# Optimization experiments

Measured on AMD Instinct MI355X. Metric: run time of the kernel, lower is better.

Reference implementation:

```python
import jax, jax.numpy as jnp
import numpy as np

N_HEAD = 16


def _rope_tables(T, head_dim, dtype):
    # RotaryEmbedding buffers: freqs = outer(t, inv_freq), half-dim tables [T, head_dim//2]
    inv_freq = 1.0 / (10000.0 ** (jnp.arange(0, head_dim, 2, dtype=jnp.float32) / head_dim))
    freqs = jnp.arange(T, dtype=jnp.float32)[:, None] * inv_freq[None, :]
    return jnp.cos(freqs).astype(dtype), jnp.sin(freqs).astype(dtype)


def _apply_rotary(x, cos, sin):
    # x: [B,H,T,D]; cos/sin: [T,D//2] broadcast over B,H
    d = x.shape[-1] // 2
    x1, x2 = x[..., :d], x[..., d:]
    return jnp.concatenate([x1 * cos - x2 * sin, x2 * cos + x1 * sin], axis=-1)


def setup_inputs() -> dict:
    key = jax.random.key(0)
    k1, k2, k3 = jax.random.split(key, 3)
    B, T, C = 2, 2048, 2048
    x = jax.random.normal(k1, (B, T, C), dtype=jnp.float32)
    Wqkv = jax.random.normal(k2, (C, 3 * C), dtype=jnp.float32) * (1.0 / np.sqrt(C))
    Wproj = jax.random.normal(k3, (C, C), dtype=jnp.float32) * (1.0 / np.sqrt(C))
    return {"x": x, "Wqkv": Wqkv, "Wproj": Wproj}


def reference(x, Wqkv, Wproj):
    B, T, C = x.shape
    H = N_HEAD
    D = C // H
    qkv = (x @ Wqkv).reshape(B, T, 3, H, D)
    q, k, v = qkv[:, :, 0], qkv[:, :, 1], qkv[:, :, 2]  # [B,T,H,D]
    q = jnp.transpose(q, (0, 2, 1, 3))  # [B,H,T,D]
    k = jnp.transpose(k, (0, 2, 1, 3))
    v = jnp.transpose(v, (0, 2, 1, 3))
    cos, sin = _rope_tables(T, D, x.dtype)
    q = _apply_rotary(q, cos, sin)
    k = _apply_rotary(k, cos, sin)
    scale = 1.0 / np.sqrt(D)
    scores = jnp.einsum('bhqd,bhkd->bhqk', q, k) * scale
    causal = jnp.tril(jnp.ones((T, T), dtype=bool))
    scores = jnp.where(causal, scores, jnp.finfo(scores.dtype).min)
    attn = jax.nn.softmax(scores, axis=-1)
    out = jnp.einsum('bhqk,bhkd->bhqd', attn, v)
    out = jnp.transpose(out, (0, 2, 1, 3)).reshape(B, T, C)
    return out @ Wproj
```

## Files before the change

kernel.cpp:

```cpp
#include <hip/hip_runtime.h>
#include <hip/hip_bf16.h>

typedef short s16b;
using bf16x4 = __attribute__((ext_vector_type(4))) short;
using bf16x8 = __attribute__((ext_vector_type(8))) short;
using f32x4  = __attribute__((ext_vector_type(4))) float;
using u32x4  = __attribute__((ext_vector_type(4))) unsigned;

#define DEVINL __device__ __forceinline__

DEVINL float bf2f(short u) {
    union { float f; unsigned u; } x;
    x.u = ((unsigned)(unsigned short)u) << 16;
    return x.f;
}
DEVINL short f2bf(float f) {
    unsigned u = __builtin_bit_cast(unsigned, f);
    u += 0x7FFFu + ((u >> 16) & 1u);
    return (short)(u >> 16);
}
DEVINL unsigned cvtpk(float a, float b) {
    unsigned r;
    asm("v_cvt_pk_bf16_f32 %0, %1, %2" : "=v"(r) : "v"(a), "v"(b));
    return r;
}

DEVINL f32x4 mfma16(bf16x8 a, bf16x8 b, f32x4 c) {
    return __builtin_amdgcn_mfma_f32_16x16x32_bf16(a, b, c, 0, 0, 0);
}

DEVINL void gload_lds16(const void* g, void* lds_uniform) {
    __builtin_amdgcn_global_load_lds(
        (const __attribute__((address_space(1))) char*)(const char*)g,
        (__attribute__((address_space(3))) char*)(char*)lds_uniform, 16, 0, 0);
}

DEVINL int perm32(int k) {
    return ((k >> 2) & 3) * 8 + ((k >> 4) & 1) * 4 + (k & 3);
}

DEVINL bf16x8 lds128(const s16b* base, int row, int ks, int g) {
    const char* p = (const char*)base + row * 128 + ((((ks << 2) + g) ^ (row & 7)) << 4);
    return *(const bf16x8*)p;
}
DEVINL bf16x8 lds256(const s16b* base, int row, int ds, int g) {
    const char* p = (const char*)base + row * 256 + ((((ds << 2) + g) ^ (row & 7)) << 4);
    return *(const bf16x8*)p;
}

__global__ void k_tables(float* __restrict__ ctab, float* __restrict__ stab) {
    int idx = blockIdx.x * 256 + threadIdx.x;
    int i = idx & 63, t = idx >> 6;
    float inv = powf(10000.0f, -(float)i * (1.0f / 64.0f));
    float fr = (float)t * inv;
    ctab[idx] = cosf(fr);
    stab[idx] = sinf(fr);
}

__global__ void k_cvt_x(const float* __restrict__ x, s16b* __restrict__ xb) {
    int idx = blockIdx.x * 256 + threadIdx.x;
    int p = idx * 4;
    int row = p >> 11, pc = p & 2047;
    int grp = pc >> 5, sp = pc & 31;
    int c = sp >> 3, half = (sp >> 2) & 1;
    int ksrc = grp * 32 + half * 16 + c * 4;
    float4 v = *(const float4*)(x + (size_t)row * 2048 + ksrc);
    bf16x4 o;
    o[0] = f2bf(v.x); o[1] = f2bf(v.y); o[2] = f2bf(v.z); o[3] = f2bf(v.w);
    *(bf16x4*)(xb + (size_t)row * 2048 + pc) = o;
}

__global__ void k_tcvt(const float* __restrict__ in, s16b* __restrict__ out, int R, int C) {
    __shared__ float tile[32][33];
    int tx = threadIdx.x & 31, ty = threadIdx.x >> 5;
    int c0 = blockIdx.x * 32, r0 = blockIdx.y * 32;
#pragma unroll
    for (int kk = 0; kk < 4; ++kk) {
        int r = ty + kk * 8;
        tile[r][tx] = in[(size_t)(r0 + r) * C + c0 + tx];
    }
    __syncthreads();
#pragma unroll
    for (int kk = 0; kk < 4; ++kk) {
        int r = ty + kk * 8;
        out[(size_t)(c0 + r) * R + r0 + perm32(tx)] = f2bf(tile[tx][r]);
    }
}

#define STG_B01(DB, KB)                                                        \
  gload_lds16(srcB + (KB), lds + 49152 + (DB) * 32768 + tid16);                \
  gload_lds16(srcB + 262144 + (KB), lds + 49152 + (DB) * 32768 + 8192 + tid16);
#define STG_B23(DB, KB)                                                        \
  gload_lds16(srcB + 524288 + (KB), lds + 49152 + (DB) * 32768 + 16384 + tid16); \
  gload_lds16(srcB + 786432 + (KB), lds + 49152 + (DB) * 32768 + 24576 + tid16);
#define STG_A01(DB, KB)                                                        \
  gload_lds16(srcA + (KB), lds + (DB) * 16384 + tid16);                        \
  gload_lds16(srcA + 262144 + (KB), lds + (DB) * 16384 + 8192 + tid16);

#define AF_READ(B, KS)                                                         \
    _Pragma("unroll")                                                          \
    for (int fi = 0; fi < 4; ++fi) {                                           \
      int row = (fi >> 1) * 64 + wm * 32 + (fi & 1) * 16 + r15;                \
      af[fi] = *(const bf16x8*)(lds + (B) * 16384 + row * 128                  \
               + ((((KS) * 4 + g) ^ (row & 7)) << 4));                         \
    }

#define PH4(B, KH, JH, STGC, WN)                                               \
  {                                                                            \
    if ((JH) == 0) { AF_READ(B, KH) }                                          \
    _Pragma("unroll")                                                          \
    for (int fj = 0; fj < 2; ++fj) {                                           \
      int row = (JH) * 128 + wn * 32 + fj * 16 + r15;                          \
      bfr[fj] = *(const bf16x8*)(lds + 49152 + (B) * 32768 + row * 128         \
                + ((((KH) * 4 + g) ^ (row & 7)) << 4));                        \
    }                                                                          \
    STGC                                                                       \
    if ((WN) == 6) { asm volatile("s_waitcnt vmcnt(6)" ::: "memory");          \
                     __builtin_amdgcn_sched_barrier(0); }                      \
    else if ((WN) == 0) { asm volatile("s_waitcnt vmcnt(0)" ::: "memory");     \
                     __builtin_amdgcn_sched_barrier(0); }                      \
    __builtin_amdgcn_s_barrier();                                              \
    asm volatile("s_waitcnt lgkmcnt(0)" ::: "memory");                         \
    __builtin_amdgcn_sched_barrier(0);                                         \
    __builtin_amdgcn_s_setprio(1);                                             \
    _Pragma("unroll")                                                          \
    for (int fi = 0; fi < 4; ++fi)                                             \
      _Pragma("unroll")                                                        \
      for (int fj = 0; fj < 2; ++fj)                                           \
        acc[fi][(JH) * 2 + fj] = mfma16(af[fi], bfr[fj], acc[fi][(JH) * 2 + fj]); \
    __builtin_amdgcn_s_setprio(0);                                             \
    __builtin_amdgcn_s_barrier();                                              \
    __builtin_amdgcn_sched_barrier(0);                                         \
  }

#define DO_TILE3(B, S1, S2, S3, WNL)                                           \
    PH4(B, 0, 0, S1, -1)                                                       \
    PH4(B, 0, 1, S2, -1)                                                       \
    PH4(B, 1, 0, S3, -1)                                                       \
    PH4(B, 1, 1, , WNL)

#define GEMM3_MAINLOOP(A_, B_)                                                 \
    __shared__ __attribute__((aligned(16))) char lds[147456];                  \
    const int tid = threadIdx.x;                                               \
    const int lane = tid & 63, wave = tid >> 6;                                \
    const int g = lane >> 4, r15 = lane & 15;                                  \
    const int wm = wave >> 2, wn = wave & 3;                                   \
    const int tid16 = tid << 4;                                                \
    const int rowL = tid16 >> 7;                                               \
    const int swzL = ((((tid16 >> 4) & 7) ^ (rowL & 7)) << 4);                 \
    const char* srcA = (const char*)(A_) + (size_t)(bm + rowL) * 4096 + swzL;  \
    const char* srcB = (const char*)(B_) + (size_t)(bn + rowL) * 4096 + swzL;  \
    f32x4 acc[4][4] = {};                                                      \
    bf16x8 af[4], bfr[2];                                                      \
    STG_B01(0, 0) STG_A01(0, 0) STG_B23(0, 0)                                  \
    STG_B01(1, 128) STG_A01(1, 128) STG_B23(1, 128)                            \
    asm volatile("s_waitcnt vmcnt(6)" ::: "memory");                           \
    __builtin_amdgcn_sched_barrier(0);                                         \
    __builtin_amdgcn_s_barrier();                                              \
    for (int t3 = 0; t3 < 10; ++t3) {                                          \
        const int kb2 = (3 * t3 + 2) * 128;                                    \
        const int kb3 = kb2 + 128, kb4 = kb2 + 256;                            \
        DO_TILE3(0, STG_B01(2, kb2), STG_A01(2, kb2), STG_B23(2, kb2), 6)      \
        DO_TILE3(1, STG_B01(0, kb3), STG_A01(0, kb3), STG_B23(0, kb3), 6)      \
        DO_TILE3(2, STG_B01(1, kb4), STG_A01(1, kb4), STG_B23(1, kb4), 6)      \
    }                                                                          \
    DO_TILE3(0, , , , 0)                                                       \
    DO_TILE3(1, , , , -1)

__global__ __launch_bounds__(512) void k_gemm_qkv(
    const s16b* __restrict__ A, const s16b* __restrict__ Bt,
    s16b* __restrict__ Qb, s16b* __restrict__ Kp, s16b* __restrict__ Vt,
    const float* __restrict__ ctab, const float* __restrict__ stab) {
    const int bid = blockIdx.x;
    const int xcd = bid & 7, local = bid >> 3;
    const int rr_ = local >> 5, w = local & 31;
    const int bm = ((xcd & 3) * 8 + (w >> 2)) * 128;
    const int bn = ((xcd >> 2) * 12 + rr_ * 4 + (w & 3)) * 256;
    GEMM3_MAINLOOP(A, Bt)
    const int which = bn >> 11;
    if (which < 2) {
        char* sml = (char*)lds;
#pragma unroll
        for (int i = 0; i < 4; ++i) {
#pragma unroll
            for (int j = 0; j < 4; ++j) {
                int mb0 = (i >> 1) * 64 + wm * 32 + (i & 1) * 16 + 4 * g;
                int nn = (j >> 1) * 128 + wn * 32 + (j & 1) * 16 + r15;
#pragma unroll
                for (int e = 0; e < 4; ++e) {
                    int mm = mb0 + e;
                    *(s16b*)(sml + mm * 528 + ((nn * 2) ^ ((mm & 3) << 5))) =
                        f2bf(acc[i][j][e]);
                }
            }
        }
        __syncthreads();
        const int mrow = tid >> 2, c4 = tid & 3;
        const int bb = bm >> 11;
        const int tt = (bm & 2047) + mrow;
        const char* srow = sml + mrow * 528;
        const int sw = (mrow & 3) << 5;
        bf16x8 v[8];
#pragma unroll
        for (int k = 0; k < 8; ++k) {
            int lc = c4 + 4 * k;
            v[k] = *(const bf16x8*)(srow + ((lc * 16) ^ sw));
        }
        float cs[2][8], sn[2][8];
#pragma unroll
        for (int j = 0; j < 2; ++j) {
            int d0 = 8 * c4 + 32 * j;
            const float* cp = ctab + tt * 64 + d0;
            const float* sp = stab + tt * 64 + d0;
            *(float4*)&cs[j][0] = *(const float4*)cp;
            *(float4*)&cs[j][4] = *(const float4*)(cp + 4);
            *(float4*)&sn[j][0] = *(const float4*)sp;
            *(float4*)&sn[j][4] = *(const float4*)(sp + 4);
        }
        if (which == 0) {
            const float SC = 0.12751744154f;
#pragma unroll
            for (int j = 0; j < 2; ++j)
#pragma unroll
                for (int e = 0; e < 8; ++e) { cs[j][e] *= SC; sn[j][e] *= SC; }
        }
        bf16x8 o[8];
#pragma unroll
        for (int hh = 0; hh < 2; ++hh)
#pragma unroll
            for (int j = 0; j < 2; ++j) {
                int kl = hh * 4 + j, kh = kl + 2;
                bf16x8 r1, r2;
#pragma unroll
                for (int e = 0; e < 8; ++e) {
                    float c = cs[j][e], s = sn[j][e];
                    float x1 = bf2f(v[kl][e]), x2 = bf2f(v[kh][e]);
                    r1[e] = f2bf(x1 * c - x2 * s);
                    r2[e] = f2bf(x2 * c + x1 * s);
                }
                o[kl] = r1; o[kh] = r2;
            }
        if (which == 0) {
#pragma unroll
            for (int k = 0; k < 8; ++k) {
                int lc = c4 + 4 * k;
                int ng = bn + lc * 8;
                int h = (ng >> 7) & 15, d = ng & 127;
                *(bf16x8*)(Qb + ((size_t)(bb * 16 + h) * 2048 + tt) * 128 + d) = o[k];
            }
        } else {
#pragma unroll
            for (int k = 0; k < 8; ++k) {
                int lc = c4 + 4 * k;
                int ng = bn + lc * 8;
                int h = (ng >> 7) & 15, d = ng & 127;
                size_t base = ((size_t)(bb * 16 + h) * 2048 + tt) * 128 + (d & ~31);
                int w2 = d & 31;
                bf16x4 lo, hi;
#pragma unroll
                for (int e = 0; e < 4; ++e) { lo[e] = o[k][e]; hi[e] = o[k][e + 4]; }
                *(bf16x4*)(Kp + base + perm32(w2)) = lo;
                *(bf16x4*)(Kp + base + perm32(w2 + 4)) = hi;
            }
        }
    } else {
#pragma unroll
        for (int i = 0; i < 4; ++i) {
            int m0 = bm + (i >> 1) * 64 + wm * 32 + (i & 1) * 16 + 4 * g;
            int b = m0 >> 11, t0 = m0 & 2047;
            int pt = (t0 & ~31) + perm32(t0 & 31);
#pragma unroll
            for (int j = 0; j < 4; ++j) {
                int n = bn + (j >> 1) * 128 + wn * 32 + (j & 1) * 16 + r15;
                int h = (n >> 7) & 15, d = n & 127;
                size_t base = ((size_t)(b * 16 + h) * 128 + d) * 2048 + pt;
                bf16x4 pk;
#pragma unroll
                for (int e = 0; e < 4; ++e) pk[e] = f2bf(acc[i][j][e]);
                *(bf16x4*)(Vt + base) = pk;
            }
        }
    }
}

__global__ __launch_bounds__(512) void k_gemm_proj(
    const s16b* __restrict__ A, const s16b* __restrict__ Bt, float* __restrict__ Co) {
    const int bid = blockIdx.x;
    const int xcd = bid & 7, local = bid >> 3;
    const int bm = (xcd * 4 + (local & 3)) * 128;
    const int bn = (local >> 2) * 256;
    GEMM3_MAINLOOP(A, Bt)
#pragma unroll
    for (int i = 0; i < 4; ++i) {
        int m0 = bm + (i >> 1) * 64 + wm * 32 + (i & 1) * 16 + 4 * g;
#pragma unroll
        for (int j = 0; j < 4; ++j) {
            int n = bn + (j >> 1) * 128 + wn * 32 + (j & 1) * 16 + r15;
#pragma unroll
            for (int e = 0; e < 4; ++e) Co[(size_t)(m0 + e) * 2048 + n] = acc[i][j][e];
        }
    }
}

__global__ __launch_bounds__(256) void k_attn(
    const s16b* __restrict__ Qb, const s16b* __restrict__ Kp,
    const s16b* __restrict__ Vt, s16b* __restrict__ AO) {
    __shared__ alignas(16) s16b Ks[64 * 128];
    __shared__ alignas(16) s16b Vs[128 * 64];
    const int tid = threadIdx.x;
    const int lane = tid & 63, wave = tid >> 6;
    const int g = lane >> 4, r15 = lane & 15;
    const int bh = blockIdx.x;
    const int qt = (blockIdx.y < 8) ? (15 - (int)blockIdx.y) : ((int)blockIdx.y - 8);
    const int q0 = qt * 128 + wave * 32;
    const s16b* Qg = Qb + (size_t)bh * 2048 * 128;
    const char* Kg = (const char*)(Kp + (size_t)bh * 2048 * 128);
    const char* Vg = (const char*)(Vt + (size_t)bh * 128 * 2048);

    bf16x8 qf[2][4];
#pragma unroll
    for (int qs = 0; qs < 2; ++qs)
#pragma unroll
        for (int ds = 0; ds < 4; ++ds) {
            const s16b* p = Qg + (size_t)(q0 + qs * 16 + r15) * 128 + ds * 32 + 4 * g;
            bf16x4 lo = *(const bf16x4*)p;
            bf16x4 hi = *(const bf16x4*)(p + 16);
            qf[qs][ds] = __builtin_shufflevector(lo, hi, 0, 1, 2, 3, 4, 5, 6, 7);
        }

    f32x4 ot[8][2] = {};
    float m_s[2] = {-3e38f, -3e38f};
    float l_s[2] = {0.f, 0.f};

    const int ktiles = qt * 2 + 2;
    for (int kt = 0; kt < ktiles; ++kt) {
        const int k0 = kt * 64;
        __syncthreads();
#pragma unroll
        for (int rr = 0; rr < 4; ++rr) {
            int uo = (rr * 256 + wave * 64) * 16;
            int o = uo + lane * 16;
            {
                int row = o >> 8, sl = (o >> 4) & 15;
                int sg = (sl ^ (row & 7)) << 4;
                gload_lds16(Kg + (size_t)(k0 + row) * 256 + sg, (char*)Ks + uo);
            }
            {
                int row = o >> 7, sl = (o >> 4) & 7;
                int sg = (sl ^ (row & 7)) << 4;
                gload_lds16(Vg + (size_t)row * 4096 + (size_t)k0 * 2 + sg, (char*)Vs + uo);
            }
        }
        __syncthreads();

        if (k0 <= q0 + 31) {
            f32x4 st[4][2] = {};
            __builtin_amdgcn_s_setprio(1);
#pragma unroll
            for (int ds = 0; ds < 4; ++ds) {
#pragma unroll
                for (int ks = 0; ks < 4; ++ks) {
                    bf16x8 kf = lds256(Ks, ks * 16 + r15, ds, g);
#pragma unroll
                    for (int qs = 0; qs < 2; ++qs)
                        st[ks][qs] = mfma16(kf, qf[qs][ds], st[ks][qs]);
                }
            }
            __builtin_amdgcn_s_setprio(0);
            if (k0 + 63 > q0) {
#pragma unroll
                for (int ks = 0; ks < 4; ++ks)
#pragma unroll
                    for (int qs = 0; qs < 2; ++qs)
#pragma unroll
                        for (int e = 0; e < 4; ++e) {
                            int kk = k0 + ks * 16 + 4 * g + e;
                            int qq = q0 + qs * 16 + r15;
                            if (kk > qq) st[ks][qs][e] = -3e38f;
                        }
            }
#pragma unroll
            for (int qs = 0; qs < 2; ++qs) {
                float mx = st[0][qs][0];
#pragma unroll
                for (int ks = 0; ks < 4; ++ks)
#pragma unroll
                    for (int e = 0; e < 4; ++e)
                        if (ks | e) mx = fmaxf(mx, st[ks][qs][e]);
                mx = fmaxf(mx, __shfl_xor(mx, 16));
                mx = fmaxf(mx, __shfl_xor(mx, 32));
                if (__any(mx > m_s[qs] + 8.f)) {
                    float mn = fmaxf(m_s[qs], mx);
                    float sf = exp2f(m_s[qs] - mn);
                    m_s[qs] = mn;
                    l_s[qs] *= sf;
#pragma unroll
                    for (int d8 = 0; d8 < 8; ++d8)
#pragma unroll
                        for (int e = 0; e < 4; ++e) ot[d8][qs][e] *= sf;
                }
                float mm = m_s[qs], sum = 0.f;
#pragma unroll
                for (int ks = 0; ks < 4; ++ks)
#pragma unroll
                    for (int e = 0; e < 4; ++e) {
                        float p = exp2f(st[ks][qs][e] - mm);
                        st[ks][qs][e] = p;
                        sum += p;
                    }
                l_s[qs] += sum;
            }
            bf16x8 pb[2][2];
#pragma unroll
            for (int k2 = 0; k2 < 2; ++k2)
#pragma unroll
                for (int qs = 0; qs < 2; ++qs) {
                    u32x4 t;
                    t[0] = cvtpk(st[2 * k2][qs][0], st[2 * k2][qs][1]);
                    t[1] = cvtpk(st[2 * k2][qs][2], st[2 * k2][qs][3]);
                    t[2] = cvtpk(st[2 * k2 + 1][qs][0], st[2 * k2 + 1][qs][1]);
                    t[3] = cvtpk(st[2 * k2 + 1][qs][2], st[2 * k2 + 1][qs][3]);
                    pb[k2][qs] = __builtin_bit_cast(bf16x8, t);
                }
            __builtin_amdgcn_s_setprio(1);
#pragma unroll
            for (int k2 = 0; k2 < 2; ++k2)
#pragma unroll
                for (int d8 = 0; d8 < 8; ++d8) {
                    bf16x8 vf = lds128(Vs, d8 * 16 + r15, k2, g);
#pragma unroll
                    for (int qs = 0; qs < 2; ++qs)
                        ot[d8][qs] = mfma16(vf, pb[k2][qs], ot[d8][qs]);
                }
            __builtin_amdgcn_s_setprio(0);
        }
    }
    int b = bh >> 4, h = bh & 15;
#pragma unroll
    for (int qs = 0; qs < 2; ++qs) {
        float l = l_s[qs];
        l += __shfl_xor(l, 16);
        l += __shfl_xor(l, 32);
        float inv = 1.0f / l;
        int q = q0 + qs * 16 + r15;
#pragma unroll
        for (int d8 = 0; d8 < 8; ++d8) {
            uint2 pk2;
            pk2.x = cvtpk(ot[d8][qs][0] * inv, ot[d8][qs][1] * inv);
            pk2.y = cvtpk(ot[d8][qs][2] * inv, ot[d8][qs][3] * inv);
            size_t off = ((size_t)(b * 2048 + q)) * 2048
                       + h * 128 + (d8 >> 1) * 32 + g * 8 + (d8 & 1) * 4;
            *(uint2*)(AO + off) = pk2;
        }
    }
}

extern "C" void kernel_launch(void* const* d_in, const int* in_sizes, int n_in,
                              void* d_out, int out_size, void* d_ws, size_t ws_size,
                              hipStream_t stream) {
    const float* x = (const float*)d_in[0];
    const float* Wqkv = (const float*)d_in[1];
    const float* Wproj = (const float*)d_in[2];
    float* out = (float*)d_out;

    char* ws = (char*)d_ws;
    float* ctab = (float*)ws;
    float* stab = ctab + 2048 * 64;
    size_t off = 1048576;
    s16b* xb = (s16b*)(ws + off); off += 16777216;
    s16b* wqkvt = (s16b*)(ws + off); off += 25165824;
    s16b* wprojt = (s16b*)(ws + off); off += 8388608;
    s16b* Qb = (s16b*)(ws + off); off += 16777216;
    s16b* Kp = (s16b*)(ws + off); off += 16777216;
    s16b* Vt = (s16b*)(ws + off); off += 16777216;
    s16b* AO = xb;

    k_tables<<<dim3(512), dim3(256), 0, stream>>>(ctab, stab);
    k_cvt_x<<<dim3(8192), dim3(256), 0, stream>>>(x, xb);
    k_tcvt<<<dim3(192, 64), dim3(256), 0, stream>>>(Wqkv, wqkvt, 2048, 6144);
    k_tcvt<<<dim3(64, 64), dim3(256), 0, stream>>>(Wproj, wprojt, 2048, 2048);
    k_gemm_qkv<<<dim3(768), dim3(512), 0, stream>>>(xb, wqkvt, Qb, Kp, Vt, ctab, stab);
    k_attn<<<dim3(32, 16), dim3(256), 0, stream>>>(Qb, Kp, Vt, AO);
    k_gemm_proj<<<dim3(256), dim3(512), 0, stream>>>(AO, wprojt, out);
}
```

Baseline: 274.1 us.

## Double-buffer K/V tiles and pair causal query tiles per attention block

The attention kernel now double-buffers the K and V shared-memory tiles, issuing the async global-to-LDS loads for the next key tile before computing on the current one and using explicit vmcnt waits plus barriers. Each block also processes two query tiles (qt and 15-qt), which evens out the causal work per block and halves the grid to 256 blocks. The intent is to hide load latency behind the MFMA work and to balance the triangular workload. In exchange it doubles LDS use, which may lower occupancy, and with fewer blocks the 256 CUs may be less well filled.

```diff
diff --git a/kernel.cpp b/kernel.cpp
--- a/kernel.cpp
+++ b/kernel.cpp
@@ -305,154 +305,180 @@
 __global__ __launch_bounds__(256) void k_attn(
     const s16b* __restrict__ Qb, const s16b* __restrict__ Kp,
     const s16b* __restrict__ Vt, s16b* __restrict__ AO) {
-    __shared__ alignas(16) s16b Ks[64 * 128];
-    __shared__ alignas(16) s16b Vs[128 * 64];
+    __shared__ alignas(16) s16b Ks[2][64 * 128];
+    __shared__ alignas(16) s16b Vs[2][128 * 64];
     const int tid = threadIdx.x;
     const int lane = tid & 63, wave = tid >> 6;
     const int g = lane >> 4, r15 = lane & 15;
-    const int bh = blockIdx.x;
-    const int qt = (blockIdx.y < 8) ? (15 - (int)blockIdx.y) : ((int)blockIdx.y - 8);
-    const int q0 = qt * 128 + wave * 32;
+    const int bh = blockIdx.x, pp = blockIdx.y;
     const s16b* Qg = Qb + (size_t)bh * 2048 * 128;
     const char* Kg = (const char*)(Kp + (size_t)bh * 2048 * 128);
     const char* Vg = (const char*)(Vt + (size_t)bh * 128 * 2048);
-
-    bf16x8 qf[2][4];
-#pragma unroll
-    for (int qs = 0; qs < 2; ++qs)
-#pragma unroll
-        for (int ds = 0; ds < 4; ++ds) {
-            const s16b* p = Qg + (size_t)(q0 + qs * 16 + r15) * 128 + ds * 32 + 4 * g;
-            bf16x4 lo = *(const bf16x4*)p;
-            bf16x4 hi = *(const bf16x4*)(p + 16);
-            qf[qs][ds] = __builtin_shufflevector(lo, hi, 0, 1, 2, 3, 4, 5, 6, 7);
-        }
-
-    f32x4 ot[8][2] = {};
-    float m_s[2] = {-3e38f, -3e38f};
-    float l_s[2] = {0.f, 0.f};
-
-    const int ktiles = qt * 2 + 2;
-    for (int kt = 0; kt < ktiles; ++kt) {
-        const int k0 = kt * 64;
-        __syncthreads();
-#pragma unroll
-        for (int rr = 0; rr < 4; ++rr) {
-            int uo = (rr * 256 + wave * 64) * 16;
-            int o = uo + lane * 16;
-            {
-                int row = o >> 8, sl = (o >> 4) & 15;
-                int sg = (sl ^ (row & 7)) << 4;
-                gload_lds16(Kg + (size_t)(k0 + row) * 256 + sg, (char*)Ks + uo);
-            }
-            {
-                int row = o >> 7, sl = (o >> 4) & 7;
-                int sg = (sl ^ (row & 7)) << 4;
-                gload_lds16(Vg + (size_t)row * 4096 + (size_t)k0 * 2 + sg, (char*)Vs + uo);
-            }
-        }
-        __syncthreads();
-
-        if (k0 <= q0 + 31) {
-            f32x4 st[4][2] = {};
-            __builtin_amdgcn_s_setprio(1);
+    const int b = bh >> 4, h = bh & 15;
+
+#define ASTG(BUF, KT)                                                          \
+    {                                                                          \
+      const int k0s = (KT) * 64;                                               \
+      _Pragma("unroll")                                                        \
+      for (int rr = 0; rr < 4; ++rr) {                                         \
+        int uo = (rr * 256 + wave * 64) * 16;                                  \
+        int o = uo + lane * 16;                                                \
+        {                                                                      \
+          int row = o >> 8, sl = (o >> 4) & 15;                                \
+          int sg = (sl ^ (row & 7)) << 4;                                      \
+          gload_lds16(Kg + (size_t)(k0s + row) * 256 + sg,                     \
+                      (char*)Ks + (BUF) * 16384 + uo);                         \
+        }                                                                      \
+        {                                                                      \
+          int row = o >> 7, sl = (o >> 4) & 7;                                 \
+          int sg = (sl ^ (row & 7)) << 4;                                      \
+          gload_lds16(Vg + (size_t)row * 4096 + (size_t)k0s * 2 + sg,          \
+                      (char*)Vs + (BUF) * 16384 + uo);                         \
+        }                                                                      \
+      }                                                                        \
+    }
+
+    for (int pass = 0; pass < 2; ++pass) {
+        const int qt = pass ? pp : (15 - pp);
+        const int q0 = qt * 128 + wave * 32;
+        const int ktiles = qt * 2 + 2;
+
+        ASTG(0, 0)
+
+        bf16x8 qf[2][4];
+#pragma unroll
+        for (int qs = 0; qs < 2; ++qs)
 #pragma unroll
             for (int ds = 0; ds < 4; ++ds) {
-#pragma unroll
-                for (int ks = 0; ks < 4; ++ks) {
-                    bf16x8 kf = lds256(Ks, ks * 16 + r15, ds, g);
-#pragma unroll
-                    for (int qs = 0; qs < 2; ++qs)
-                        st[ks][qs] = mfma16(kf, qf[qs][ds], st[ks][qs]);
+                const s16b* p = Qg + (size_t)(q0 + qs * 16 + r15) * 128 + ds * 32 + 4 * g;
+                bf16x4 lo = *(const bf16x4*)p;
+                bf16x4 hi = *(const bf16x4*)(p + 16);
+                qf[qs][ds] = __builtin_shufflevector(lo, hi, 0, 1, 2, 3, 4, 5, 6, 7);
+            }
+
+        f32x4 ot[8][2] = {};
+        float m_s[2] = {-3e38f, -3e38f};
+        float l_s[2] = {0.f, 0.f};
+
+        for (int kt = 0; kt < ktiles; ++kt) {
+            const int k0 = kt * 64;
+            if (kt + 1 < ktiles) {
+                ASTG((kt + 1) & 1, kt + 1)
+                asm volatile("s_waitcnt vmcnt(8)" ::: "memory");
+            } else {
+                asm volatile("s_waitcnt vmcnt(0)" ::: "memory");
+            }
+            __builtin_amdgcn_sched_barrier(0);
+            __builtin_amdgcn_s_barrier();
+            asm volatile("" ::: "memory");
+            __builtin_amdgcn_sched_barrier(0);
+
+            if (k0 <= q0 + 31) {
+                const s16b* Kb_ = (const s16b*)((const char*)Ks + (kt & 1) * 16384);
+                const s16b* Vb_ = (const s16b*)((const char*)Vs + (kt & 1) * 16384);
+                f32x4 st[4][2] = {};
+                __builtin_amdgcn_s_setprio(1);
+#pragma unroll
+                for (int ds = 0; ds < 4; ++ds) {
+#pragma unroll
+                    for (int ks = 0; ks < 4; ++ks) {
+                        bf16x8 kf = lds256(Kb_, ks * 16 + r15, ds, g);
+#pragma unroll
+                        for (int qs = 0; qs < 2; ++qs)
+                            st[ks][qs] = mfma16(kf, qf[qs][ds], st[ks][qs]);
+                    }
                 }
-            }
-            __builtin_amdgcn_s_setprio(0);
-            if (k0 + 63 > q0) {
-#pragma unroll
-                for (int ks = 0; ks < 4; ++ks)
-#pragma unroll
-                    for (int qs = 0; qs < 2; ++qs)
+                __builtin_amdgcn_s_setprio(0);
+                if (k0 + 63 > q0) {
+#pragma unroll
+                    for (int ks = 0; ks < 4; ++ks)
+#pragma unroll
+                        for (int qs = 0; qs < 2; ++qs)
+#pragma unroll
+                            for (int e = 0; e < 4; ++e) {
+                                int kk = k0 + ks * 16 + 4 * g + e;
+                                int qq = q0 + qs * 16 + r15;
+                                if (kk > qq) st[ks][qs][e] = -3e38f;
+                            }
+                }
+#pragma unroll
+                for (int qs = 0; qs < 2; ++qs) {
+                    float mx = st[0][qs][0];
+#pragma unroll
+                    for (int ks = 0; ks < 4; ++ks)
+#pragma unroll
+                        for (int e = 0; e < 4; ++e)
+                            if (ks | e) mx = fmaxf(mx, st[ks][qs][e]);
+                    mx = fmaxf(mx, __shfl_xor(mx, 16));
+                    mx = fmaxf(mx, __shfl_xor(mx, 32));
+                    if (__any(mx > m_s[qs] + 8.f)) {
+                        float mn = fmaxf(m_s[qs], mx);
+                        float sf = exp2f(m_s[qs] - mn);
+                        m_s[qs] = mn;
+                        l_s[qs] *= sf;
+#pragma unroll
+                        for (int d8 = 0; d8 < 8; ++d8)
+#pragma unroll
+                            for (int e = 0; e < 4; ++e) ot[d8][qs][e] *= sf;
+                    }
+                    float mm = m_s[qs], sum = 0.f;
+#pragma unroll
+                    for (int ks = 0; ks < 4; ++ks)
 #pragma unroll
                         for (int e = 0; e < 4; ++e) {
-                            int kk = k0 + ks * 16 + 4 * g + e;
-                            int qq = q0 + qs * 16 + r15;
-                            if (kk > qq) st[ks][qs][e] = -3e38f;
+                            float p = exp2f(st[ks][qs][e] - mm);
+                            st[ks][qs][e] = p;
+                            sum += p;
                         }
-            }
-#pragma unroll
-            for (int qs = 0; qs < 2; ++qs) {
-                float mx = st[0][qs][0];
-#pragma unroll
-                for (int ks = 0; ks < 4; ++ks)
-#pragma unroll
-                    for (int e = 0; e < 4; ++e)
-                        if (ks | e) mx = fmaxf(mx, st[ks][qs][e]);
-                mx = fmaxf(mx, __shfl_xor(mx, 16));
-                mx = fmaxf(mx, __shfl_xor(mx, 32));
-                if (__any(mx > m_s[qs] + 8.f)) {
-                    float mn = fmaxf(m_s[qs], mx);
-                    float sf = exp2f(m_s[qs] - mn);
-                    m_s[qs] = mn;
-                    l_s[qs] *= sf;
-#pragma unroll
-                    for (int d8 = 0; d8 < 8; ++d8)
-#pragma unroll
-                        for (int e = 0; e < 4; ++e) ot[d8][qs][e] *= sf;
+                    l_s[qs] += sum;
                 }
-                float mm = m_s[qs], sum = 0.f;
-#pragma unroll
-                for (int ks = 0; ks < 4; ++ks)
-#pragma unroll
-                    for (int e = 0; e < 4; ++e) {
-                        float p = exp2f(st[ks][qs][e] - mm);
-                        st[ks][qs][e] = p;
-                        sum += p;
+                bf16x8 pb[2][2];
+#pragma unroll
+                for (int k2 = 0; k2 < 2; ++k2)
+#pragma unroll
+                    for (int qs = 0; qs < 2; ++qs) {
+                        u32x4 t;
+                        t[0] = cvtpk(st[2 * k2][qs][0], st[2 * k2][qs][1]);
+                        t[1] = cvtpk(st[2 * k2][qs][2], st[2 * k2][qs][3]);
+                        t[2] = cvtpk(st[2 * k2 + 1][qs][0], st[2 * k2 + 1][qs][1]);
+                        t[3] = cvtpk(st[2 * k2 + 1][qs][2], st[2 * k2 + 1][qs][3]);
+                        pb[k2][qs] = __builtin_bit_cast(bf16x8, t);
                     }
-                l_s[qs] += sum;
-            }
-            bf16x8 pb[2][2];
-#pragma unroll
-            for (int k2 = 0; k2 < 2; ++k2)
-#pragma unroll
-                for (int qs = 0; qs < 2; ++qs) {
-                    u32x4 t;
-                    t[0] = cvtpk(st[2 * k2][qs][0], st[2 * k2][qs][1]);
-                    t[1] = cvtpk(st[2 * k2][qs][2], st[2 * k2][qs][3]);
-                    t[2] = cvtpk(st[2 * k2 + 1][qs][0], st[2 * k2 + 1][qs][1]);
-                    t[3] = cvtpk(st[2 * k2 + 1][qs][2], st[2 * k2 + 1][qs][3]);
-                    pb[k2][qs] = __builtin_bit_cast(bf16x8, t);
-                }
-            __builtin_amdgcn_s_setprio(1);
-#pragma unroll
-            for (int k2 = 0; k2 < 2; ++k2)
-#pragma unroll
-                for (int d8 = 0; d8 < 8; ++d8) {
-                    bf16x8 vf = lds128(Vs, d8 * 16 + r15, k2, g);
-#pragma unroll
-                    for (int qs = 0; qs < 2; ++qs)
-                        ot[d8][qs] = mfma16(vf, pb[k2][qs], ot[d8][qs]);
-                }
-            __builtin_amdgcn_s_setprio(0);
-        }
-    }
-    int b = bh >> 4, h = bh & 15;
-#pragma unroll
-    for (int qs = 0; qs < 2; ++qs) {
-        float l = l_s[qs];
-        l += __shfl_xor(l, 16);
-        l += __shfl_xor(l, 32);
-        float inv = 1.0f / l;
-        int q = q0 + qs * 16 + r15;
-#pragma unroll
-        for (int d8 = 0; d8 < 8; ++d8) {
-            uint2 pk2;
-            pk2.x = cvtpk(ot[d8][qs][0] * inv, ot[d8][qs][1] * inv);
-            pk2.y = cvtpk(ot[d8][qs][2] * inv, ot[d8][qs][3] * inv);
-            size_t off = ((size_t)(b * 2048 + q)) * 2048
-                       + h * 128 + (d8 >> 1) * 32 + g * 8 + (d8 & 1) * 4;
-            *(uint2*)(AO + off) = pk2;
-        }
-    }
+                __builtin_amdgcn_s_setprio(1);
+#pragma unroll
+                for (int k2 = 0; k2 < 2; ++k2)
+#pragma unroll
+                    for (int d8 = 0; d8 < 8; ++d8) {
+                        bf16x8 vf = lds128(Vb_, d8 * 16 + r15, k2, g);
+#pragma unroll
+                        for (int qs = 0; qs < 2; ++qs)
+                            ot[d8][qs] = mfma16(vf, pb[k2][qs], ot[d8][qs]);
+                    }
+                __builtin_amdgcn_s_setprio(0);
+            }
+            asm volatile("" ::: "memory");
+            __builtin_amdgcn_sched_barrier(0);
+            __builtin_amdgcn_s_barrier();
+        }
+#pragma unroll
+        for (int qs = 0; qs < 2; ++qs) {
+            float l = l_s[qs];
+            l += __shfl_xor(l, 16);
+            l += __shfl_xor(l, 32);
+            float inv = 1.0f / l;
+            int q = q0 + qs * 16 + r15;
+#pragma unroll
+            for (int d8 = 0; d8 < 8; ++d8) {
+                uint2 pk2;
+                pk2.x = cvtpk(ot[d8][qs][0] * inv, ot[d8][qs][1] * inv);
+                pk2.y = cvtpk(ot[d8][qs][2] * inv, ot[d8][qs][3] * inv);
+                size_t off = ((size_t)(b * 2048 + q)) * 2048
+                           + h * 128 + (d8 >> 1) * 32 + g * 8 + (d8 & 1) * 4;
+                *(uint2*)(AO + off) = pk2;
+            }
+        }
+    }
+#undef ASTG
 }
 
 extern "C" void kernel_launch(void* const* d_in, const int* in_sizes, int n_in,
@@ -480,6 +506,6 @@
     k_tcvt<<<dim3(192, 64), dim3(256), 0, stream>>>(Wqkv, wqkvt, 2048, 6144);
     k_tcvt<<<dim3(64, 64), dim3(256), 0, stream>>>(Wproj, wprojt, 2048, 2048);
     k_gemm_qkv<<<dim3(768), dim3(512), 0, stream>>>(xb, wqkvt, Qb, Kp, Vt, ctab, stab);
-    k_attn<<<dim3(32, 16), dim3(256), 0, stream>>>(Qb, Kp, Vt, AO);
+    k_attn<<<dim3(32, 8), dim3(256), 0, stream>>>(Qb, Kp, Vt, AO);
     k_gemm_proj<<<dim3(256), dim3(512), 0, stream>>>(AO, wprojt, out);
 }
```

Measured after the change: 260.1 us. -5.1%, faster.
